# Kernel tuning notes

Measured on AMD Instinct MI355X. Metric: run time of the kernel, lower is better.

Reference implementation:

```python
import jax, jax.numpy as jnp
import numpy as np

NUM_EXPERT = 8
IN_FEAT = 1024
OUT_FEAT = 1024
N_TOKENS = 8192


def setup_inputs() -> dict:
    key = jax.random.key(0)
    k_inp, k_gate, k_w = jax.random.split(key, 3)
    inp = jax.random.normal(k_inp, (N_TOKENS, IN_FEAT), dtype=jnp.float32)
    gate = jax.random.randint(k_gate, (N_TOKENS,), 0, NUM_EXPERT, dtype=jnp.int32)
    # FMoELinear weight: [num_expert, out_feat, in_feat], kaiming-uniform-like init
    bound = 1.0 / np.sqrt(IN_FEAT)
    weight = jax.random.uniform(
        k_w, (NUM_EXPERT, OUT_FEAT, IN_FEAT), dtype=jnp.float32,
        minval=-bound, maxval=bound)
    return {"inp": inp, "gate": gate, "weight": weight}


def reference(inp, gate, weight):
    # out[i] = weight[gate[i]] @ inp[i]  (top-1 MoE dispatch + grouped GEMM + combine)
    # Loop over the small fixed expert set via scan; each step does a masked
    # dense GEMM so only tokens routed to expert e contribute.
    n, _ = inp.shape
    num_expert, out_feat, _ = weight.shape

    def body(acc, ew):
        e, w_e = ew  # w_e: [out_feat, in_feat]
        mask = (gate == e).astype(inp.dtype)[:, None]  # [n, 1]
        acc = acc + (inp * mask) @ w_e.T               # [n, out_feat]
        return acc, None

    init = jnp.zeros((n, out_feat), dtype=inp.dtype)
    out, _ = jax.lax.scan(body, init, (jnp.arange(num_expert), weight))
    return out
```

## Files before the change

kernel.cpp:

```cpp
#include <hip/hip_runtime.h>
#include <hip/hip_bf16.h>

#define N_TOKENS 8192
#define IN_FEAT 1024
#define OUT_FEAT 1024
#define NUM_EXPERT 8

#define BM 128
#define BN 128
#define BK 32

typedef __bf16 bf16x8 __attribute__((ext_vector_type(8)));
typedef float f32x4 __attribute__((ext_vector_type(4)));

__device__ __forceinline__ unsigned int rne16(float x) {
    union { float f; unsigned int u; } c;
    c.f = x;
    unsigned int u = c.u;
    u += 0x7fffu + ((u >> 16) & 1u);
    return u >> 16;
}
__device__ __forceinline__ unsigned int pk2(float x, float y) {
    return rne16(x) | (rne16(y) << 16);
}

__device__ __forceinline__ void load_lds16(const void* g, void* l) {
    __builtin_amdgcn_global_load_lds(
        (const __attribute__((address_space(1))) unsigned int*)g,
        (__attribute__((address_space(3))) unsigned int*)l,
        16, 0, 0);
}

__device__ __forceinline__ void sort_block256(const int* __restrict__ gate,
                                              int* __restrict__ perm,
                                              int* __restrict__ seg) {
    __shared__ int whist[4][NUM_EXPERT];
    __shared__ int wbase[4][NUM_EXPERT];
    const int t = threadIdx.x;
    const int wave = t >> 6, lane = t & 63;
    const unsigned long long lt = (lane == 0) ? 0ull : (~0ull >> (64 - lane));

    int4 v[8];
    #pragma unroll
    for (int j = 0; j < 8; ++j)
        v[j] = ((const int4*)gate)[j * 256 + t];

    int cnt[NUM_EXPERT];
    #pragma unroll
    for (int e = 0; e < NUM_EXPERT; ++e) cnt[e] = 0;
    #pragma unroll
    for (int j = 0; j < 8; ++j) {
        #pragma unroll
        for (int q = 0; q < 4; ++q) {
            const int g = (q == 0) ? v[j].x : (q == 1) ? v[j].y
                        : (q == 2) ? v[j].z : v[j].w;
            #pragma unroll
            for (int e = 0; e < NUM_EXPERT; ++e) {
                unsigned long long m = __ballot(g == e);
                cnt[e] += (int)__popcll(m);
            }
        }
    }
    if (lane == 0) {
        #pragma unroll
        for (int e = 0; e < NUM_EXPERT; ++e) whist[wave][e] = cnt[e];
    }
    __syncthreads();

    if (t == 0) {
        int s = 0;
        #pragma unroll
        for (int e = 0; e < NUM_EXPERT; ++e) {
            seg[e] = s;
            int b = s;
            #pragma unroll
            for (int w = 0; w < 4; ++w) { wbase[w][e] = b; b += whist[w][e]; }
            s = b;
        }
        seg[NUM_EXPERT] = s;
    }
    __syncthreads();

    int off[NUM_EXPERT];
    #pragma unroll
    for (int e = 0; e < NUM_EXPERT; ++e) off[e] = wbase[wave][e];
    #pragma unroll
    for (int j = 0; j < 8; ++j) {
        #pragma unroll
        for (int q = 0; q < 4; ++q) {
            const int g = (q == 0) ? v[j].x : (q == 1) ? v[j].y
                        : (q == 2) ? v[j].z : v[j].w;
            const int tok = j * 1024 + t * 4 + q;
            #pragma unroll
            for (int e = 0; e < NUM_EXPERT; ++e) {
                unsigned long long m = __ballot(g == e);
                if (g == e) perm[off[e] + (int)__popcll(m & lt)] = tok;
                off[e] += (int)__popcll(m);
            }
        }
    }
}

__global__ __launch_bounds__(256) void moe_sort(const int* __restrict__ gate,
                                                int* __restrict__ perm,
                                                int* __restrict__ seg) {
    sort_block256(gate, perm, seg);
}

__global__ __launch_bounds__(256) void moe_prep_sort(
    const float* __restrict__ inp,
    const float* __restrict__ weight,
    const int* __restrict__ gate,
    int* __restrict__ perm,
    int* __restrict__ seg,
    unsigned int* __restrict__ A2,
    unsigned int* __restrict__ W2) {

    const int bid = blockIdx.x;
    if (bid == 0) {
        sort_block256(gate, perm, seg);
        return;
    }
    const int cid = bid - 1;
    const int t = threadIdx.x;
    const int wave = t >> 6, lane = t & 63;
    const float* src;
    unsigned int* dst;
    if (cid < 2048) {
        int row = cid * 4 + wave;
        src = inp + row * IN_FEAT;
        dst = A2 + row * (IN_FEAT / 2);
    } else {
        int row = (cid - 2048) * 4 + wave;
        src = weight + row * IN_FEAT;
        dst = W2 + row * (IN_FEAT / 2);
    }
    #pragma unroll
    for (int j = 0; j < 4; ++j) {
        float4 v = *(const float4*)(src + j * 256 + lane * 4);
        uint2 o;
        o.x = pk2(v.x, v.y);
        o.y = pk2(v.z, v.w);
        *(uint2*)(dst + j * 128 + lane * 2) = o;
    }
}

__global__ __launch_bounds__(256, 4) void moe_gemm(
    const unsigned short* __restrict__ A2,
    const unsigned short* __restrict__ W2,
    const int* __restrict__ perm,
    const int* __restrict__ seg,
    float* __restrict__ out) {

    const int bid = blockIdx.x;
    const int e = bid & 7;
    const int ntile = (bid >> 3) & 7;
    const int mtile = bid >> 6;

    const int base = seg[e];
    const int cnt = seg[e + 1] - base;
    if (mtile * BM >= cnt) return;
    const int tbase = base + mtile * BM;
    int rows = cnt - mtile * BM; if (rows > BM) rows = BM;

    __shared__ __align__(16) unsigned short lA[2][BM * BK];
    __shared__ __align__(16) unsigned short lB[2][BN * BK];

    const int t = threadIdx.x;

    const int crow = t >> 2;
    const int p = (t & 3) ^ (crow & 3);
    int ar0 = tbase + crow;       if (ar0 > N_TOKENS - 1) ar0 = N_TOKENS - 1;
    int ar1 = tbase + 64 + crow;  if (ar1 > N_TOKENS - 1) ar1 = N_TOKENS - 1;
    const int pr0 = perm[ar0];
    const int pr1 = perm[ar1];
    const unsigned short* gA0 = A2 + (size_t)pr0 * IN_FEAT + p * 8;
    const unsigned short* gA1 = A2 + (size_t)pr1 * IN_FEAT + p * 8;
    const unsigned short* gB0 = W2 + e * (OUT_FEAT * IN_FEAT)
                                + (ntile * BN + crow) * IN_FEAT + p * 8;
    const unsigned short* gB1 = gB0 + 64 * IN_FEAT;
    const int dofs = t * 8;
    const int dofs2 = (t + 256) * 8;

    const int wave = t >> 6;
    const int lane = t & 63;
    const int wm = (wave & 1) << 6;
    const int wn = (wave >> 1) << 6;
    const int l15 = lane & 15;
    const int quad = lane >> 4;
    const int qx = quad ^ (l15 & 3);
    const int fofsA = (wm + l15) * BK + qx * 8;
    const int fofsB = (wn + l15) * BK + qx * 8;

    f32x4 acc[4][4];
    #pragma unroll
    for (int i = 0; i < 4; ++i)
        #pragma unroll
        for (int j = 0; j < 4; ++j)
            acc[i][j] = (f32x4)0.0f;

    load_lds16(gA0, &lA[0][dofs]);
    load_lds16(gA1, &lA[0][dofs2]);
    load_lds16(gB0, &lB[0][dofs]);
    load_lds16(gB1, &lB[0][dofs2]);

    #pragma unroll 1
    for (int kk = 0; kk < 16; ++kk) {
        const int k0 = kk * 64;

        __syncthreads();
        load_lds16(gA0 + k0 + 32, &lA[1][dofs]);
        load_lds16(gA1 + k0 + 32, &lA[1][dofs2]);
        load_lds16(gB0 + k0 + 32, &lB[1][dofs]);
        load_lds16(gB1 + k0 + 32, &lB[1][dofs2]);

        {
            bf16x8 af[4], bq[4];
            #pragma unroll
            for (int i = 0; i < 4; ++i)
                af[i] = *(const bf16x8*)&lA[0][fofsA + i * 16 * BK];
            #pragma unroll
            for (int j = 0; j < 4; ++j)
                bq[j] = *(const bf16x8*)&lB[0][fofsB + j * 16 * BK];
            #pragma unroll
            for (int i = 0; i < 4; ++i)
                #pragma unroll
                for (int j = 0; j < 4; ++j)
                    acc[i][j] = __builtin_amdgcn_mfma_f32_16x16x32_bf16(
                        af[i], bq[j], acc[i][j], 0, 0, 0);
        }

        __syncthreads();
        if (kk < 15) {
            load_lds16(gA0 + k0 + 64, &lA[0][dofs]);
            load_lds16(gA1 + k0 + 64, &lA[0][dofs2]);
            load_lds16(gB0 + k0 + 64, &lB[0][dofs]);
            load_lds16(gB1 + k0 + 64, &lB[0][dofs2]);
        }

        {
            bf16x8 af[4], bq[4];
            #pragma unroll
            for (int i = 0; i < 4; ++i)
                af[i] = *(const bf16x8*)&lA[1][fofsA + i * 16 * BK];
            #pragma unroll
            for (int j = 0; j < 4; ++j)
                bq[j] = *(const bf16x8*)&lB[1][fofsB + j * 16 * BK];
            #pragma unroll
            for (int i = 0; i < 4; ++i)
                #pragma unroll
                for (int j = 0; j < 4; ++j)
                    acc[i][j] = __builtin_amdgcn_mfma_f32_16x16x32_bf16(
                        af[i], bq[j], acc[i][j], 0, 0, 0);
        }
    }

    #pragma unroll
    for (int mi = 0; mi < 4; ++mi) {
        #pragma unroll
        for (int r = 0; r < 4; ++r) {
            int row = wm + mi * 16 + quad * 4 + r;
            if (row < rows) {
                int token = perm[tbase + row];
                float* op = out + token * OUT_FEAT + ntile * BN + wn;
                #pragma unroll
                for (int ni = 0; ni < 4; ++ni)
                    op[ni * 16 + l15] = acc[mi][ni][r];
            }
        }
    }
}

#define FLDSW 20
__global__ __launch_bounds__(256, 4) void moe_gemm_fb(
    const float* __restrict__ inp,
    const float* __restrict__ weight,
    const int* __restrict__ perm,
    const int* __restrict__ seg,
    float* __restrict__ out) {

    const int bid = blockIdx.x;
    const int mtile = bid >> 7;
    const int e = (bid >> 4) & 7;
    const int ntile = bid & 15;

    const int base = seg[e];
    const int cnt = seg[e + 1] - base;
    if (mtile * 128 >= cnt) return;

    __shared__ unsigned int lA[128 * FLDSW];
    __shared__ unsigned int lB[64 * FLDSW];
    __shared__ int rowids[128];

    const int t = threadIdx.x;
    if (t < 128) {
        int r = mtile * 128 + t;
        rowids[t] = (r < cnt) ? perm[base + r] : -1;
    }
    __syncthreads();

    const int srow = t >> 1;
    const int scol = (t & 1) << 4;
    const int tokA = rowids[srow];
    const bool aval = (tokA >= 0);
    const float* aptr = inp + (aval ? tokA : 0) * IN_FEAT + scol;
    const int sdstA = srow * FLDSW + (scol >> 1);
    const int browB = t >> 2;
    const int bcol = (t & 3) << 3;
    const float* bptr = weight + e * (OUT_FEAT * IN_FEAT)
                        + (ntile * 64 + browB) * IN_FEAT + bcol;
    const int sdstB = browB * FLDSW + (bcol >> 1);

    const int wave = t >> 6;
    const int lane = t & 63;
    const int wm = (wave & 1) << 6;
    const int wn = (wave >> 1) << 5;
    const int l15 = lane & 15;
    const int quad = lane >> 4;

    f32x4 acc[4][2];
    #pragma unroll
    for (int i = 0; i < 4; ++i)
        #pragma unroll
        for (int j = 0; j < 2; ++j)
            acc[i][j] = (f32x4)0.0f;

    float4 ra[4], rb[2];
    {
        const float4* ap = (const float4*)aptr;
        const float4* bp = (const float4*)bptr;
        #pragma unroll
        for (int i = 0; i < 4; ++i) ra[i] = ap[i];
        #pragma unroll
        for (int i = 0; i < 2; ++i) rb[i] = bp[i];
    }

    for (int k0 = 0; k0 < IN_FEAT; k0 += 32) {
        unsigned int ua[8], ub[4];
        #pragma unroll
        for (int i = 0; i < 4; ++i) {
            ua[2 * i]     = pk2(ra[i].x, ra[i].y);
            ua[2 * i + 1] = pk2(ra[i].z, ra[i].w);
        }
        #pragma unroll
        for (int i = 0; i < 2; ++i) {
            ub[2 * i]     = pk2(rb[i].x, rb[i].y);
            ub[2 * i + 1] = pk2(rb[i].z, rb[i].w);
        }
        if (!aval) {
            #pragma unroll
            for (int i = 0; i < 8; ++i) ua[i] = 0u;
        }

        __syncthreads();
        *(uint4*)&lA[sdstA]     = make_uint4(ua[0], ua[1], ua[2], ua[3]);
        *(uint4*)&lA[sdstA + 4] = make_uint4(ua[4], ua[5], ua[6], ua[7]);
        *(uint4*)&lB[sdstB]     = make_uint4(ub[0], ub[1], ub[2], ub[3]);
        __syncthreads();

        if (k0 + 32 < IN_FEAT) {
            const float4* ap = (const float4*)(aptr + k0 + 32);
            const float4* bp = (const float4*)(bptr + k0 + 32);
            #pragma unroll
            for (int i = 0; i < 4; ++i) ra[i] = ap[i];
            #pragma unroll
            for (int i = 0; i < 2; ++i) rb[i] = bp[i];
        }

        bf16x8 af[4], bq[2];
        #pragma unroll
        for (int i = 0; i < 4; ++i)
            af[i] = *(const bf16x8*)&lA[(wm + i * 16 + l15) * FLDSW + (quad << 2)];
        #pragma unroll
        for (int j = 0; j < 2; ++j)
            bq[j] = *(const bf16x8*)&lB[(wn + j * 16 + l15) * FLDSW + (quad << 2)];

        #pragma unroll
        for (int i = 0; i < 4; ++i)
            #pragma unroll
            for (int j = 0; j < 2; ++j)
                acc[i][j] = __builtin_amdgcn_mfma_f32_16x16x32_bf16(
                    af[i], bq[j], acc[i][j], 0, 0, 0);
    }

    #pragma unroll
    for (int mi = 0; mi < 4; ++mi) {
        #pragma unroll
        for (int r = 0; r < 4; ++r) {
            int row = wm + mi * 16 + quad * 4 + r;
            int token = rowids[row];
            if (token >= 0) {
                float* op = out + token * OUT_FEAT + ntile * 64 + wn;
                #pragma unroll
                for (int ni = 0; ni < 2; ++ni)
                    op[ni * 16 + l15] = acc[mi][ni][r];
            }
        }
    }
}

extern "C" void kernel_launch(void* const* d_in, const int* in_sizes, int n_in,
                              void* d_out, int out_size, void* d_ws, size_t ws_size,
                              hipStream_t stream) {
    const float* inp = (const float*)d_in[0];
    const int* gate = (const int*)d_in[1];
    const float* weight = (const float*)d_in[2];
    float* out = (float*)d_out;

    int* perm = (int*)d_ws;
    int* seg = perm + N_TOKENS;

    const size_t need = 65536 + 2ull * N_TOKENS * IN_FEAT * 2;
    if (ws_size >= need) {
        unsigned int* A2 = (unsigned int*)((char*)d_ws + 65536);
        unsigned int* W2 = A2 + (N_TOKENS * IN_FEAT / 2);
        moe_prep_sort<<<4097, 256, 0, stream>>>(inp, weight, gate, perm, seg,
                                                A2, W2);
        moe_gemm<<<4096, 256, 0, stream>>>((const unsigned short*)A2,
                                           (const unsigned short*)W2,
                                           perm, seg, out);
    } else {
        moe_sort<<<1, 256, 0, stream>>>(gate, perm, seg);
        moe_gemm_fb<<<8192, 256, 0, stream>>>(inp, weight, perm, seg, out);
    }
}
```

Before: 142.7 us.

## Fuse fp32-to-bf16 conversion into GEMM tile loads, drop separate prep pass

Removes the separate pre-pass that converted the inputs and weights to bf16 in workspace. The GEMM now reads fp32 from global memory into registers, converts to bf16 and writes the result into double-buffered LDS, with a single barrier per K-step. This avoids writing and re-reading the bf16 copies. In exchange it gives up the direct global-to-LDS loads, doubles the global bytes read per tile, and leaves the sort as a separate serial single-block launch. It also lowers launch bounds to 2 blocks per CU.

New measurement: 157.7 us. 1.11x slower.

```diff
diff --git a/kernel.cpp b/kernel.cpp
--- a/kernel.cpp
+++ b/kernel.cpp
@@ -13,22 +13,13 @@
 typedef __bf16 bf16x8 __attribute__((ext_vector_type(8)));
 typedef float f32x4 __attribute__((ext_vector_type(4)));
 
-__device__ __forceinline__ unsigned int rne16(float x) {
-    union { float f; unsigned int u; } c;
-    c.f = x;
-    unsigned int u = c.u;
-    u += 0x7fffu + ((u >> 16) & 1u);
-    return u >> 16;
-}
-__device__ __forceinline__ unsigned int pk2(float x, float y) {
-    return rne16(x) | (rne16(y) << 16);
-}
-
-__device__ __forceinline__ void load_lds16(const void* g, void* l) {
-    __builtin_amdgcn_global_load_lds(
-        (const __attribute__((address_space(1))) unsigned int*)g,
-        (__attribute__((address_space(3))) unsigned int*)l,
-        16, 0, 0);
+__device__ __forceinline__ bf16x8 cvt8(float4 lo, float4 hi) {
+    bf16x8 r;
+    r[0] = (__bf16)lo.x; r[1] = (__bf16)lo.y;
+    r[2] = (__bf16)lo.z; r[3] = (__bf16)lo.w;
+    r[4] = (__bf16)hi.x; r[5] = (__bf16)hi.y;
+    r[6] = (__bf16)hi.z; r[7] = (__bf16)hi.w;
+    return r;
 }
 
 __device__ __forceinline__ void sort_block256(const int* __restrict__ gate,
@@ -107,47 +98,9 @@
     sort_block256(gate, perm, seg);
 }
 
-__global__ __launch_bounds__(256) void moe_prep_sort(
+__global__ __launch_bounds__(256, 2) void moe_gemm_f(
     const float* __restrict__ inp,
     const float* __restrict__ weight,
-    const int* __restrict__ gate,
-    int* __restrict__ perm,
-    int* __restrict__ seg,
-    unsigned int* __restrict__ A2,
-    unsigned int* __restrict__ W2) {
-
-    const int bid = blockIdx.x;
-    if (bid == 0) {
-        sort_block256(gate, perm, seg);
-        return;
-    }
-    const int cid = bid - 1;
-    const int t = threadIdx.x;
-    const int wave = t >> 6, lane = t & 63;
-    const float* src;
-    unsigned int* dst;
-    if (cid < 2048) {
-        int row = cid * 4 + wave;
-        src = inp + row * IN_FEAT;
-        dst = A2 + row * (IN_FEAT / 2);
-    } else {
-        int row = (cid - 2048) * 4 + wave;
-        src = weight + row * IN_FEAT;
-        dst = W2 + row * (IN_FEAT / 2);
-    }
-    #pragma unroll
-    for (int j = 0; j < 4; ++j) {
-        float4 v = *(const float4*)(src + j * 256 + lane * 4);
-        uint2 o;
-        o.x = pk2(v.x, v.y);
-        o.y = pk2(v.z, v.w);
-        *(uint2*)(dst + j * 128 + lane * 2) = o;
-    }
-}
-
-__global__ __launch_bounds__(256, 4) void moe_gemm(
-    const unsigned short* __restrict__ A2,
-    const unsigned short* __restrict__ W2,
     const int* __restrict__ perm,
     const int* __restrict__ seg,
     float* __restrict__ out) {
@@ -172,13 +125,11 @@
     const int p = (t & 3) ^ (crow & 3);
     int ar0 = tbase + crow;       if (ar0 > N_TOKENS - 1) ar0 = N_TOKENS - 1;
     int ar1 = tbase + 64 + crow;  if (ar1 > N_TOKENS - 1) ar1 = N_TOKENS - 1;
-    const int pr0 = perm[ar0];
-    const int pr1 = perm[ar1];
-    const unsigned short* gA0 = A2 + (size_t)pr0 * IN_FEAT + p * 8;
-    const unsigned short* gA1 = A2 + (size_t)pr1 * IN_FEAT + p * 8;
-    const unsigned short* gB0 = W2 + e * (OUT_FEAT * IN_FEAT)
-                                + (ntile * BN + crow) * IN_FEAT + p * 8;
-    const unsigned short* gB1 = gB0 + 64 * IN_FEAT;
+    const float* gA0 = inp + (size_t)perm[ar0] * IN_FEAT + p * 8;
+    const float* gA1 = inp + (size_t)perm[ar1] * IN_FEAT + p * 8;
+    const float* gB0 = weight + (size_t)e * (OUT_FEAT * IN_FEAT)
+                       + (ntile * BN + crow) * IN_FEAT + p * 8;
+    const float* gB1 = gB0 + 64 * IN_FEAT;
     const int dofs = t * 8;
     const int dofs2 = (t + 256) * 8;
 
@@ -199,29 +150,39 @@
         for (int j = 0; j < 4; ++j)
             acc[i][j] = (f32x4)0.0f;
 
-    load_lds16(gA0, &lA[0][dofs]);
-    load_lds16(gA1, &lA[0][dofs2]);
-    load_lds16(gB0, &lB[0][dofs]);
-    load_lds16(gB1, &lB[0][dofs2]);
+    float4 ra0, ra1, ra2, ra3, rb0, rb1, rb2, rb3;
+
+    ra0 = *(const float4*)(gA0);     ra1 = *(const float4*)(gA0 + 4);
+    ra2 = *(const float4*)(gA1);     ra3 = *(const float4*)(gA1 + 4);
+    rb0 = *(const float4*)(gB0);     rb1 = *(const float4*)(gB0 + 4);
+    rb2 = *(const float4*)(gB1);     rb3 = *(const float4*)(gB1 + 4);
+    *(bf16x8*)&lA[0][dofs]  = cvt8(ra0, ra1);
+    *(bf16x8*)&lA[0][dofs2] = cvt8(ra2, ra3);
+    *(bf16x8*)&lB[0][dofs]  = cvt8(rb0, rb1);
+    *(bf16x8*)&lB[0][dofs2] = cvt8(rb2, rb3);
 
     #pragma unroll 1
-    for (int kk = 0; kk < 16; ++kk) {
-        const int k0 = kk * 64;
+    for (int s = 0; s < 32; ++s) {
+        const int cur = s & 1;
+        const int k0 = (s + 1) * BK;
+
+        if (s < 31) {
+            ra0 = *(const float4*)(gA0 + k0);     ra1 = *(const float4*)(gA0 + k0 + 4);
+            ra2 = *(const float4*)(gA1 + k0);     ra3 = *(const float4*)(gA1 + k0 + 4);
+            rb0 = *(const float4*)(gB0 + k0);     rb1 = *(const float4*)(gB0 + k0 + 4);
+            rb2 = *(const float4*)(gB1 + k0);     rb3 = *(const float4*)(gB1 + k0 + 4);
+        }
 
         __syncthreads();
-        load_lds16(gA0 + k0 + 32, &lA[1][dofs]);
-        load_lds16(gA1 + k0 + 32, &lA[1][dofs2]);
-        load_lds16(gB0 + k0 + 32, &lB[1][dofs]);
-        load_lds16(gB1 + k0 + 32, &lB[1][dofs2]);
 
         {
             bf16x8 af[4], bq[4];
             #pragma unroll
             for (int i = 0; i < 4; ++i)
-                af[i] = *(const bf16x8*)&lA[0][fofsA + i * 16 * BK];
+                af[i] = *(const bf16x8*)&lA[cur][fofsA + i * 16 * BK];
             #pragma unroll
             for (int j = 0; j < 4; ++j)
-                bq[j] = *(const bf16x8*)&lB[0][fofsB + j * 16 * BK];
+                bq[j] = *(const bf16x8*)&lB[cur][fofsB + j * 16 * BK];
             #pragma unroll
             for (int i = 0; i < 4; ++i)
                 #pragma unroll
@@ -230,28 +191,11 @@
                         af[i], bq[j], acc[i][j], 0, 0, 0);
         }
 
-        __syncthreads();
-        if (kk < 15) {
-            load_lds16(gA0 + k0 + 64, &lA[0][dofs]);
-            load_lds16(gA1 + k0 + 64, &lA[0][dofs2]);
-            load_lds16(gB0 + k0 + 64, &lB[0][dofs]);
-            load_lds16(gB1 + k0 + 64, &lB[0][dofs2]);
-        }
-
-        {
-            bf16x8 af[4], bq[4];
-            #pragma unroll
-            for (int i = 0; i < 4; ++i)
-                af[i] = *(const bf16x8*)&lA[1][fofsA + i * 16 * BK];
-            #pragma unroll
-            for (int j = 0; j < 4; ++j)
-                bq[j] = *(const bf16x8*)&lB[1][fofsB + j * 16 * BK];
-            #pragma unroll
-            for (int i = 0; i < 4; ++i)
-                #pragma unroll
-                for (int j = 0; j < 4; ++j)
-                    acc[i][j] = __builtin_amdgcn_mfma_f32_16x16x32_bf16(
-                        af[i], bq[j], acc[i][j], 0, 0, 0);
+        if (s < 31) {
+            *(bf16x8*)&lA[cur ^ 1][dofs]  = cvt8(ra0, ra1);
+            *(bf16x8*)&lA[cur ^ 1][dofs2] = cvt8(ra2, ra3);
+            *(bf16x8*)&lB[cur ^ 1][dofs]  = cvt8(rb0, rb1);
+            *(bf16x8*)&lB[cur ^ 1][dofs2] = cvt8(rb2, rb3);
         }
     }
 
@@ -271,134 +215,6 @@
     }
 }
 
-#define FLDSW 20
-__global__ __launch_bounds__(256, 4) void moe_gemm_fb(
-    const float* __restrict__ inp,
-    const float* __restrict__ weight,
-    const int* __restrict__ perm,
-    const int* __restrict__ seg,
-    float* __restrict__ out) {
-
-    const int bid = blockIdx.x;
-    const int mtile = bid >> 7;
-    const int e = (bid >> 4) & 7;
-    const int ntile = bid & 15;
-
-    const int base = seg[e];
-    const int cnt = seg[e + 1] - base;
-    if (mtile * 128 >= cnt) return;
-
-    __shared__ unsigned int lA[128 * FLDSW];
-    __shared__ unsigned int lB[64 * FLDSW];
-    __shared__ int rowids[128];
-
-    const int t = threadIdx.x;
-    if (t < 128) {
-        int r = mtile * 128 + t;
-        rowids[t] = (r < cnt) ? perm[base + r] : -1;
-    }
-    __syncthreads();
-
-    const int srow = t >> 1;
-    const int scol = (t & 1) << 4;
-    const int tokA = rowids[srow];
-    const bool aval = (tokA >= 0);
-    const float* aptr = inp + (aval ? tokA : 0) * IN_FEAT + scol;
-    const int sdstA = srow * FLDSW + (scol >> 1);
-    const int browB = t >> 2;
-    const int bcol = (t & 3) << 3;
-    const float* bptr = weight + e * (OUT_FEAT * IN_FEAT)
-                        + (ntile * 64 + browB) * IN_FEAT + bcol;
-    const int sdstB = browB * FLDSW + (bcol >> 1);
-
-    const int wave = t >> 6;
-    const int lane = t & 63;
-    const int wm = (wave & 1) << 6;
-    const int wn = (wave >> 1) << 5;
-    const int l15 = lane & 15;
-    const int quad = lane >> 4;
-
-    f32x4 acc[4][2];
-    #pragma unroll
-    for (int i = 0; i < 4; ++i)
-        #pragma unroll
-        for (int j = 0; j < 2; ++j)
-            acc[i][j] = (f32x4)0.0f;
-
-    float4 ra[4], rb[2];
-    {
-        const float4* ap = (const float4*)aptr;
-        const float4* bp = (const float4*)bptr;
-        #pragma unroll
-        for (int i = 0; i < 4; ++i) ra[i] = ap[i];
-        #pragma unroll
-        for (int i = 0; i < 2; ++i) rb[i] = bp[i];
-    }
-
-    for (int k0 = 0; k0 < IN_FEAT; k0 += 32) {
-        unsigned int ua[8], ub[4];
-        #pragma unroll
-        for (int i = 0; i < 4; ++i) {
-            ua[2 * i]     = pk2(ra[i].x, ra[i].y);
-            ua[2 * i + 1] = pk2(ra[i].z, ra[i].w);
-        }
-        #pragma unroll
-        for (int i = 0; i < 2; ++i) {
-            ub[2 * i]     = pk2(rb[i].x, rb[i].y);
-            ub[2 * i + 1] = pk2(rb[i].z, rb[i].w);
-        }
-        if (!aval) {
-            #pragma unroll
-            for (int i = 0; i < 8; ++i) ua[i] = 0u;
-        }
-
-        __syncthreads();
-        *(uint4*)&lA[sdstA]     = make_uint4(ua[0], ua[1], ua[2], ua[3]);
-        *(uint4*)&lA[sdstA + 4] = make_uint4(ua[4], ua[5], ua[6], ua[7]);
-        *(uint4*)&lB[sdstB]     = make_uint4(ub[0], ub[1], ub[2], ub[3]);
-        __syncthreads();
-
-        if (k0 + 32 < IN_FEAT) {
-            const float4* ap = (const float4*)(aptr + k0 + 32);
-            const float4* bp = (const float4*)(bptr + k0 + 32);
-            #pragma unroll
-            for (int i = 0; i < 4; ++i) ra[i] = ap[i];
-            #pragma unroll
-            for (int i = 0; i < 2; ++i) rb[i] = bp[i];
-        }
-
-        bf16x8 af[4], bq[2];
-        #pragma unroll
-        for (int i = 0; i < 4; ++i)
-            af[i] = *(const bf16x8*)&lA[(wm + i * 16 + l15) * FLDSW + (quad << 2)];
-        #pragma unroll
-        for (int j = 0; j < 2; ++j)
-            bq[j] = *(const bf16x8*)&lB[(wn + j * 16 + l15) * FLDSW + (quad << 2)];
-
-        #pragma unroll
-        for (int i = 0; i < 4; ++i)
-            #pragma unroll
-            for (int j = 0; j < 2; ++j)
-                acc[i][j] = __builtin_amdgcn_mfma_f32_16x16x32_bf16(
-                    af[i], bq[j], acc[i][j], 0, 0, 0);
-    }
-
-    #pragma unroll
-    for (int mi = 0; mi < 4; ++mi) {
-        #pragma unroll
-        for (int r = 0; r < 4; ++r) {
-            int row = wm + mi * 16 + quad * 4 + r;
-            int token = rowids[row];
-            if (token >= 0) {
-                float* op = out + token * OUT_FEAT + ntile * 64 + wn;
-                #pragma unroll
-                for (int ni = 0; ni < 2; ++ni)
-                    op[ni * 16 + l15] = acc[mi][ni][r];
-            }
-        }
-    }
-}
-
 extern "C" void kernel_launch(void* const* d_in, const int* in_sizes, int n_in,
                               void* d_out, int out_size, void* d_ws, size_t ws_size,
                               hipStream_t stream) {
@@ -410,17 +226,6 @@
     int* perm = (int*)d_ws;
     int* seg = perm + N_TOKENS;
 
-    const size_t need = 65536 + 2ull * N_TOKENS * IN_FEAT * 2;
-    if (ws_size >= need) {
-        unsigned int* A2 = (unsigned int*)((char*)d_ws + 65536);
-        unsigned int* W2 = A2 + (N_TOKENS * IN_FEAT / 2);
-        moe_prep_sort<<<4097, 256, 0, stream>>>(inp, weight, gate, perm, seg,
-                                                A2, W2);
-        moe_gemm<<<4096, 256, 0, stream>>>((const unsigned short*)A2,
-                                           (const unsigned short*)W2,
-                                           perm, seg, out);
-    } else {
-        moe_sort<<<1, 256, 0, stream>>>(gate, perm, seg);
-        moe_gemm_fb<<<8192, 256, 0, stream>>>(inp, weight, perm, seg, out);
-    }
-}
+    moe_sort<<<1, 256, 0, stream>>>(gate, perm, seg);
+    moe_gemm_f<<<4096, 256, 0, stream>>>(inp, weight, perm, seg, out);
+}
```
